# Performance work log

Measured on AMD Instinct MI355X. Metric: run time of the kernel, lower is better.

Reference implementation:

```python
import jax, jax.numpy as jnp
import numpy as np

N = 4096          # samples
D_FEAT = 256      # embedding dim
N_CLASSES = 64
N_NEIGHBORS = 3


def _sq_dists(x):
    # torch.cdist(x, x, p=2).pow(2): squared euclidean pairwise distances
    x2 = jnp.sum(x * x, axis=1)
    d = x2[:, None] + x2[None, :] - 2.0 * (x @ x.T)
    return jnp.maximum(d, 0.0)


def setup_inputs() -> dict:
    key = jax.random.key(0)
    k1, k2 = jax.random.split(key)
    outputs = jax.random.normal(k1, (N, D_FEAT), dtype=jnp.float32)
    label_inds = jax.random.randint(k2, (N,), 0, N_CLASSES)
    return {"outputs": outputs, "label_inds": label_inds, "n_neighbors": N_NEIGHBORS}


def reference(outputs, label_inds, n_neighbors):
    n = outputs.shape[0]
    D = _sq_dists(outputs)                                    # [n, n]

    # _select_targets: per-class k-NN == masked global k-NN (same squared dists)
    same = label_inds[:, None] == label_inds[None, :]
    eye = jnp.eye(n, dtype=bool)
    dd = jnp.where(same & ~eye, D, jnp.inf)
    _, tn = jax.lax.top_k(-dd, n_neighbors)                   # [n, k] target neighbors (global idx)

    target_d = jnp.take_along_axis(D, tn, axis=1)             # [n, k]
    pull = jnp.sum(target_d)
    margin_radii = 1.0 + jnp.max(target_d, axis=1)            # [n]

    # mask: True everywhere except target neighbors and the diagonal
    rows = jnp.arange(n)[:, None]
    mask = jnp.ones((n, n), dtype=bool).at[rows, tn].set(False) & ~eye

    # Original broadcast (max_dist [n,1] vs distance [n,1,n]) yields
    #   push = sum_i sum_{a,j} relu(margin_radii[i] - D[a,j]) * mask[a,j]
    # i.e. each r_i is compared against ALL masked distances. Compute this
    # O(n^3)-element sum exactly in O(n^2 log n) via sort + prefix sums:
    #   sum_d relu(r - d) = r * #{d < r} - sum_{d < r} d
    d_flat = jnp.where(mask.reshape(-1), D.reshape(-1), jnp.inf)
    d_sorted = jnp.sort(d_flat)
    csum = jnp.cumsum(jnp.where(jnp.isinf(d_sorted), 0.0, d_sorted))
    csum0 = jnp.concatenate([jnp.zeros((1,), D.dtype), csum])
    counts = jnp.searchsorted(d_sorted, margin_radii, side='left')  # strict d < r
    push = jnp.sum(margin_radii * counts.astype(D.dtype) - csum0[counts])

    return (pull + push) / n
```

## Files before the change

### kernel.cpp

```cpp
#include <hip/hip_runtime.h>
#include <hip/hip_bf16.h>
#include <float.h>

#define N 4096
#define DF 256
#define NBINS2 4096
#define MAXM 128
#define NPUSHBLK 528

typedef __attribute__((ext_vector_type(8))) short short8v;
typedef __attribute__((ext_vector_type(8))) unsigned short ushort8v;
typedef __attribute__((ext_vector_type(4))) float floatx4;

__device__ inline unsigned short f2bf(float f) {
    __hip_bfloat16 h = __float2bfloat16(f);
    return *reinterpret_cast<unsigned short*>(&h);
}
__device__ inline float bf2f(unsigned short h) {
    unsigned int u = ((unsigned int)h) << 16;
    return __uint_as_float(u);
}

__device__ inline void gload_lds16(const void* g, void* l) {
    __builtin_amdgcn_global_load_lds((const __attribute__((address_space(1))) void*)g,
                                     (__attribute__((address_space(3))) void*)l, 16, 0, 0);
}

__global__ __launch_bounds__(256) void prep_kernel(const float* __restrict__ X,
                                                   const int* __restrict__ labels,
                                                   float* __restrict__ x2,
                                                   __hip_bfloat16* __restrict__ Xb,
                                                   int* __restrict__ cnt,
                                                   int* __restrict__ members,
                                                   double* __restrict__ accd,
                                                   unsigned int* __restrict__ ticket,
                                                   int useXb) {
    int t = threadIdx.x;
    if (blockIdx.x == 1024) {
        __shared__ int scnt[64];
        if (t < 8) accd[t] = 0.0;
        if (t == 8) *ticket = 0u;
        if (t < 64) scnt[t] = 0;
        __syncthreads();
        for (int i = t; i < N; i += 256) {
            int c = labels[i];
            int pos = atomicAdd(&scnt[c], 1);
            if (pos < MAXM) members[(c << 8) + pos] = i;
        }
        __syncthreads();
        if (t < 64) cnt[t] = min(scnt[t], MAXM);
        return;
    }
    int row = blockIdx.x * 4 + (t >> 6);
    int l = t & 63;
    int idx = row * 64 + l;
    float4 v = ((const float4*)X)[idx];
    if (useXb) {
        ushort4 o;
        o.x = f2bf(v.x); o.y = f2bf(v.y); o.z = f2bf(v.z); o.w = f2bf(v.w);
        ((ushort4*)Xb)[idx] = o;
    }
    float s = v.x * v.x + v.y * v.y + v.z * v.z + v.w * v.w;
#pragma unroll
    for (int off = 32; off > 0; off >>= 1) s += __shfl_xor(s, off, 64);
    if (l == 0) x2[row] = s;
}

__device__ inline void top3_upd(float& b0, float& b1, float& b2, float dd) {
    if (dd < b2) {
        if (dd < b1) { b2 = b1; if (dd < b0) { b1 = b0; b0 = dd; } else b1 = dd; }
        else b2 = dd;
    }
}

__global__ __launch_bounds__(512) void knn_mfma_kernel(const float* __restrict__ X,
                                                       const float* __restrict__ x2,
                                                       const int* __restrict__ cnt,
                                                       const int* __restrict__ members,
                                                       float* __restrict__ radii,
                                                       float* __restrict__ targetd) {
    __shared__ __align__(16) char smem[131072];
    __shared__ int marr[MAXM];
    __shared__ float mx2[MAXM];

    int c = blockIdx.x;
    int m = cnt[c];
    int tid = threadIdx.x;
    int lane = tid & 63;
    int wid = tid >> 6;
    const int* mem = members + (c << 8);

    if (tid < MAXM) {
        int mi = (tid < m) ? mem[tid] : -1;
        marr[tid] = mi;
        mx2[tid] = (mi >= 0) ? x2[mi] : 0.f;
    }
    __syncthreads();

    int RB = (m + 15) >> 4;
    char* Hi = smem;
    char* Lo = smem + 65536;

    for (int idx = tid; idx < RB * 512; idx += 512) {
        int rb = idx >> 9;
        int rem = idx & 511;
        int kb = rem >> 4;
        int r0 = rem & 15;
        int row = rb * 16 + r0;
        ushort8v vhi = (ushort8v){0,0,0,0,0,0,0,0};
        ushort8v vlo = vhi;
        if (row < m) {
            const float4* src = (const float4*)(X + (size_t)marr[row] * DF + kb * 8);
            float4 u0 = src[0], u1 = src[1];
            float uu[8] = {u0.x, u0.y, u0.z, u0.w, u1.x, u1.y, u1.z, u1.w};
#pragma unroll
            for (int p = 0; p < 8; ++p) {
                unsigned short h = f2bf(uu[p]);
                vhi[p] = h;
                vlo[p] = f2bf(uu[p] - bf2f(h));
            }
        }
        *((ushort8v*)(Hi + ((size_t)idx << 4))) = vhi;
        *((ushort8v*)(Lo + ((size_t)idx << 4))) = vlo;
    }
    __syncthreads();

    if (wid >= RB) return;

    short8v aHi[8], aLo[8];
#pragma unroll
    for (int kk = 0; kk < 8; ++kk) {
        size_t off = (size_t)wid * 8192 + (size_t)kk * 1024 + ((size_t)lane << 4);
        aHi[kk] = *((const short8v*)(Hi + off));
        aLo[kk] = *((const short8v*)(Lo + off));
    }

    int g = lane >> 4;
    int cl = lane & 15;
    float x2i[4];
#pragma unroll
    for (int r = 0; r < 4; ++r) {
        int il = wid * 16 + g * 4 + r;
        x2i[r] = (il < MAXM) ? mx2[il] : 0.f;
    }

    float t0[4], t1[4], t2[4];
#pragma unroll
    for (int r = 0; r < 4; ++r) { t0[r] = FLT_MAX; t1[r] = FLT_MAX; t2[r] = FLT_MAX; }

    for (int ct = 0; ct < RB; ++ct) {
        floatx4 acc = (floatx4){0.f, 0.f, 0.f, 0.f};
#pragma unroll
        for (int kk = 0; kk < 8; ++kk) {
            size_t off = (size_t)ct * 8192 + (size_t)kk * 1024 + ((size_t)lane << 4);
            short8v bHi = *((const short8v*)(Hi + off));
            short8v bLo = *((const short8v*)(Lo + off));
            acc = __builtin_amdgcn_mfma_f32_16x16x32_bf16(aLo[kk], bHi, acc, 0, 0, 0);
            acc = __builtin_amdgcn_mfma_f32_16x16x32_bf16(aHi[kk], bLo, acc, 0, 0, 0);
            acc = __builtin_amdgcn_mfma_f32_16x16x32_bf16(aHi[kk], bHi, acc, 0, 0, 0);
        }
        int jl = ct * 16 + cl;
        float x2j = (jl < MAXM) ? mx2[jl] : 0.f;
#pragma unroll
        for (int r = 0; r < 4; ++r) {
            int il = wid * 16 + g * 4 + r;
            float d = fmaxf(x2i[r] + x2j - 2.f * acc[r], 0.f);
            bool valid = (jl < m) && (il < m) && (jl != il);
            top3_upd(t0[r], t1[r], t2[r], valid ? d : FLT_MAX);
        }
    }

#pragma unroll
    for (int off = 1; off <= 8; off <<= 1) {
#pragma unroll
        for (int r = 0; r < 4; ++r) {
            float c0 = __shfl_xor(t0[r], off, 64);
            float c1 = __shfl_xor(t1[r], off, 64);
            float c2 = __shfl_xor(t2[r], off, 64);
            float m0, m1, m2;
            if (t0[r] <= c0) {
                m0 = t0[r];
                if (t1[r] <= c0) { m1 = t1[r]; m2 = fminf(t2[r], c0); }
                else { m1 = c0; m2 = fminf(t1[r], c1); }
            } else {
                m0 = c0;
                if (c1 <= t0[r]) { m1 = c1; m2 = fminf(c2, t0[r]); }
                else { m1 = t0[r]; m2 = fminf(c1, t1[r]); }
            }
            t0[r] = m0; t1[r] = m1; t2[r] = m2;
        }
    }
    if (cl == 0) {
#pragma unroll
        for (int r = 0; r < 4; ++r) {
            int il = wid * 16 + g * 4 + r;
            if (il < m) {
                int gi = marr[il];
                targetd[3 * gi + 0] = t0[r];
                targetd[3 * gi + 1] = t1[r];
                targetd[3 * gi + 2] = t2[r];
                radii[gi] = 1.f + t2[r];
            }
        }
    }
}

__global__ __launch_bounds__(1024) void histo_ftab_kernel(const float* __restrict__ radii,
                                                          const float* __restrict__ targetd,
                                                          float2* __restrict__ ftab_g,
                                                          float* __restrict__ hdr,
                                                          double* __restrict__ accd) {
    __shared__ int cntb[NBINS2];
    __shared__ float sumb[NBINS2];
    __shared__ float fv[NBINS2 + 1];
    __shared__ float aux[64];
    __shared__ int iaux[16];
    int t = threadIdx.x;
    int wid = t >> 6, lane = t & 63;

    float4 vv = ((const float4*)radii)[t];
    float v0 = vv.x, v1 = vv.y, v2 = vv.z, v3 = vv.w;

    float mn = fminf(fminf(v0, v1), fminf(v2, v3));
    float mx = fmaxf(fmaxf(v0, v1), fmaxf(v2, v3));
#pragma unroll
    for (int off = 32; off > 0; off >>= 1) {
        mn = fminf(mn, __shfl_xor(mn, off, 64));
        mx = fmaxf(mx, __shfl_xor(mx, off, 64));
    }
    if (lane == 0) { aux[wid] = mn; aux[wid + 16] = mx; }
    cntb[t] = 0; cntb[t + 1024] = 0; cntb[t + 2048] = 0; cntb[t + 3072] = 0;
    sumb[t] = 0.f; sumb[t + 1024] = 0.f; sumb[t + 2048] = 0.f; sumb[t + 3072] = 0.f;
    __syncthreads();
    mn = aux[0]; mx = aux[16];
    for (int w = 1; w < 16; ++w) { mn = fminf(mn, aux[w]); mx = fmaxf(mx, aux[w + 16]); }
    float range = fmaxf(mx - mn, 1e-30f);
    float scale = (float)NBINS2 / range * (1.f - 1e-6f);

    int b0i = max(0, min((int)((v0 - mn) * scale), NBINS2 - 1));
    int b1i = max(0, min((int)((v1 - mn) * scale), NBINS2 - 1));
    int b2i = max(0, min((int)((v2 - mn) * scale), NBINS2 - 1));
    int b3i = max(0, min((int)((v3 - mn) * scale), NBINS2 - 1));
    atomicAdd(&cntb[b0i], 1); atomicAdd(&sumb[b0i], v0);
    atomicAdd(&cntb[b1i], 1); atomicAdd(&sumb[b1i], v1);
    atomicAdd(&cntb[b2i], 1); atomicAdd(&sumb[b2i], v2);
    atomicAdd(&cntb[b3i], 1); atomicAdd(&sumb[b3i], v3);
    __syncthreads();

    int c0 = cntb[4 * t], c1 = cntb[4 * t + 1], c2 = cntb[4 * t + 2], c3 = cntb[4 * t + 3];
    float s0 = sumb[4 * t], s1 = sumb[4 * t + 1], s2 = sumb[4 * t + 2], s3 = sumb[4 * t + 3];
    int toti = c0 + c1 + c2 + c3;
    float totf = s0 + s1 + s2 + s3;
    int sci = toti;
    float scf = totf;
#pragma unroll
    for (int off = 1; off < 64; off <<= 1) {
        int yi = __shfl_down(sci, off, 64);
        float yf = __shfl_down(scf, off, 64);
        if (lane + off < 64) { sci += yi; scf += yf; }
    }
    if (lane == 0) { iaux[wid] = sci; aux[wid] = scf; }
    __syncthreads();
    if (t < 16) {
        int xi = iaux[t];
        float xf = aux[t];
        int si = xi;
        float sf = xf;
#pragma unroll
        for (int off = 1; off < 16; off <<= 1) {
            int yi = __shfl_down(si, off, 64);
            float yf = __shfl_down(sf, off, 64);
            if (t + off < 16) { si += yi; sf += yf; }
        }
        iaux[t] = si - xi;
        aux[t] = sf - xf;
    }
    __syncthreads();
    int afteri = iaux[wid] + (sci - toti);
    float afterf = aux[wid] + (scf - totf);
    int C3 = c3 + afteri, C2 = c2 + C3, C1 = c1 + C2, C0 = c0 + C1;
    float S3 = s3 + afterf, S2 = s2 + S3, S1 = s1 + S2, S0 = s0 + S1;

    float wbin = range / (float)NBINS2;
    {
        float x0 = mn + wbin * (float)(4 * t);
        fv[4 * t + 0] = S0 - x0 * (float)C0;
        float x1 = mn + wbin * (float)(4 * t + 1);
        fv[4 * t + 1] = S1 - x1 * (float)C1;
        float x2e = mn + wbin * (float)(4 * t + 2);
        fv[4 * t + 2] = S2 - x2e * (float)C2;
        float x3 = mn + wbin * (float)(4 * t + 3);
        fv[4 * t + 3] = S3 - x3 * (float)C3;
    }
    if (t == 0) fv[NBINS2] = 0.f;
    __syncthreads();

    for (int b = t; b < NBINS2; b += 1024)
        ftab_g[b] = make_float2(fv[b], fv[b + 1] - fv[b]);
    float Stot = fv[0] + mn * (float)N;
    if (t == 0) {
        hdr[0] = mn;
        hdr[1] = mx;
        hdr[2] = (float)NBINS2 / fmaxf(mx - mn, 1e-20f);
        hdr[3] = Stot;
    }

    float invw = (float)NBINS2 / fmaxf(mx - mn, 1e-20f);
    float loc = 0.f, pul = 0.f;
    for (int idx = t; idx < 3 * N; idx += 1024) {
        float d = targetd[idx];
        pul += d;
        if (d >= mx) continue;
        if (d < mn) {
            loc += fmaf(-d, (float)N, Stot);
        } else {
            float tpos = (d - mn) * invw;
            int b = min((int)tpos, NBINS2 - 1);
            float frac = tpos - (float)b;
            loc += fmaf(frac, fv[b + 1] - fv[b], fv[b]);
        }
    }
#pragma unroll
    for (int off = 32; off > 0; off >>= 1) {
        loc += __shfl_xor(loc, off, 64);
        pul += __shfl_xor(pul, off, 64);
    }
    __syncthreads();
    if (lane == 0) { aux[wid] = loc; aux[wid + 16] = pul; }
    __syncthreads();
    if (t == 0) {
        float s = 0.f, p = 0.f;
        for (int w = 0; w < 16; ++w) { s += aux[w]; p += aux[w + 16]; }
        accd[2] = (double)s;
        accd[0] = (double)p;
    }
}

template<int USEXB>
__global__ __launch_bounds__(256) void push_gemm_kernel(const float* __restrict__ X,
                                                        const __hip_bfloat16* __restrict__ Xb,
                                                        const float* __restrict__ x2,
                                                        const float2* __restrict__ ftab_g,
                                                        const float* __restrict__ hdr,
                                                        float* __restrict__ pp,
                                                        unsigned int* __restrict__ ticket,
                                                        const double* __restrict__ accd,
                                                        float* __restrict__ out) {
    __shared__ __align__(16) char smem[32768];
    __shared__ float x2r[128], x2c[128];
    __shared__ float red[256];
    __shared__ double wsumD[4];
    __shared__ int lastFlag;

    int bid = blockIdx.x;
    int by = 0, rem = bid;
    while (rem >= 32 - by) { rem -= 32 - by; ++by; }
    int bx = by + rem;
    int rowBase = by * 128, colBase = bx * 128;

    int tid = threadIdx.x;
    int lane = tid & 63;
    int wv = tid >> 6;
    int wy = wv >> 1, wx = wv & 1;

    floatx4 acc4[4][4];
#pragma unroll
    for (int m = 0; m < 4; ++m)
#pragma unroll
        for (int n = 0; n < 4; ++n) acc4[m][n] = (floatx4){0.f, 0.f, 0.f, 0.f};

    if (tid < 128) { x2r[tid] = x2[rowBase + tid]; x2c[tid] = x2[colBase + tid]; }

    for (int k0 = 0; k0 < DF; k0 += 64) {
        if (k0) __syncthreads();
        if (USEXB) {
            const __hip_bfloat16* Ab = Xb + (size_t)rowBase * DF;
            const __hip_bfloat16* Bb = Xb + (size_t)colBase * DF;
#pragma unroll
            for (int i = 0; i < 4; ++i) {
                int did = wv * 256 + i * 64 + lane;
                int row = ((did >> 7) << 4) | (did & 15);
                int kb = (did >> 4) & 7;
                size_t goff = (size_t)row * DF + k0 + kb * 8;
                char* ldsA = smem + (size_t)(wv * 256 + i * 64) * 16;
                gload_lds16(Ab + goff, ldsA);
                gload_lds16(Bb + goff, ldsA + 16384);
            }
        } else {
#pragma unroll
            for (int cch = 0; cch < 4; ++cch) {
                int did = tid + (cch << 8);
                int row = ((did >> 7) << 4) | (did & 15);
                int kb = (did >> 4) & 7;
                const float* srcA = X + (size_t)(rowBase + row) * DF + k0 + kb * 8;
                const float* srcB = X + (size_t)(colBase + row) * DF + k0 + kb * 8;
                float4 a0 = *(const float4*)srcA;
                float4 a1 = *(const float4*)(srcA + 4);
                float4 e0 = *(const float4*)srcB;
                float4 e1 = *(const float4*)(srcB + 4);
                ushort8v va, vb;
                va[0] = f2bf(a0.x); va[1] = f2bf(a0.y); va[2] = f2bf(a0.z); va[3] = f2bf(a0.w);
                va[4] = f2bf(a1.x); va[5] = f2bf(a1.y); va[6] = f2bf(a1.z); va[7] = f2bf(a1.w);
                vb[0] = f2bf(e0.x); vb[1] = f2bf(e0.y); vb[2] = f2bf(e0.z); vb[3] = f2bf(e0.w);
                vb[4] = f2bf(e1.x); vb[5] = f2bf(e1.y); vb[6] = f2bf(e1.z); vb[7] = f2bf(e1.w);
                *((ushort8v*)(smem + (did << 4))) = va;
                *((ushort8v*)(smem + 16384 + (did << 4))) = vb;
            }
        }
        __syncthreads();
#pragma unroll
        for (int kk = 0; kk < 2; ++kk) {
            short8v a[4], b[4];
#pragma unroll
            for (int m = 0; m < 4; ++m)
                a[m] = *((const short8v*)(smem + (((wy * 4 + m) * 2 + kk) << 10) + (lane << 4)));
#pragma unroll
            for (int n = 0; n < 4; ++n)
                b[n] = *((const short8v*)(smem + 16384 + (((wx * 4 + n) * 2 + kk) << 10) + (lane << 4)));
#pragma unroll
            for (int m = 0; m < 4; ++m)
#pragma unroll
                for (int n = 0; n < 4; ++n)
                    acc4[m][n] = __builtin_amdgcn_mfma_f32_16x16x32_bf16(a[m], b[n], acc4[m][n], 0, 0, 0);
        }
    }
    __syncthreads();

    float4* ft4 = (float4*)smem;
    for (int i = tid; i < 2048; i += 256) ft4[i] = ((const float4*)ftab_g)[i];
    __syncthreads();
    const float2* ftab = (const float2*)smem;
    float d0v = hdr[0], rmaxv = hdr[1], invw = hdr[2], Stot = hdr[3];
    bool diag = (by == bx);

    float local = 0.f;
    int g = lane >> 4;
    int cl = lane & 15;
#pragma unroll
    for (int m = 0; m < 4; ++m) {
#pragma unroll
        for (int n = 0; n < 4; ++n) {
            floatx4 v = acc4[m][n];
            int gcl = wx * 64 + n * 16 + cl;
            float x2cv = x2c[gcl];
#pragma unroll
            for (int r = 0; r < 4; ++r) {
                int grl = wy * 64 + m * 16 + g * 4 + r;
                if (diag && grl == gcl) continue;
                float d = fmaxf(x2r[grl] + x2cv - 2.f * v[r], 0.f);
                if (d >= rmaxv) continue;
                if (d < d0v) {
                    local += fmaf(-d, (float)N, Stot);
                } else {
                    float tpos = (d - d0v) * invw;
                    int b = min((int)tpos, NBINS2 - 1);
                    float frac = tpos - (float)b;
                    float2 ab = ftab[b];
                    local += fmaf(frac, ab.y, ab.x);
                }
            }
        }
    }
    red[tid] = local;
    __syncthreads();
    for (int s2 = 128; s2 > 0; s2 >>= 1) {
        if (tid < s2) red[tid] += red[tid + s2];
        __syncthreads();
    }
    if (tid == 0) {
        float wt = diag ? 1.f : 2.f;
        pp[bid] = wt * red[0];
        __threadfence();
        unsigned int old = atomicAdd(ticket, 1u);
        lastFlag = (old == NPUSHBLK - 1) ? 1 : 0;
    }
    __syncthreads();

    if (lastFlag) {
        __threadfence();
        double s = 0.0;
        for (int i = tid; i < NPUSHBLK; i += 256) s += (double)pp[i];
#pragma unroll
        for (int off = 32; off > 0; off >>= 1) s += __shfl_down(s, off, 64);
        if (lane == 0) wsumD[wv] = s;
        __syncthreads();
        if (tid == 0) {
            double tot = wsumD[0] + wsumD[1] + wsumD[2] + wsumD[3];
            out[0] = (float)((accd[0] + tot - accd[2]) / (double)N);
        }
    }
}

extern "C" void kernel_launch(void* const* d_in, const int* in_sizes, int n_in,
                              void* d_out, int out_size, void* d_ws, size_t ws_size,
                              hipStream_t stream) {
    const float* X = (const float*)d_in[0];
    const int* labels = (const int*)d_in[1];
    float* out = (float*)d_out;

    char* w = (char*)d_ws;
    double* accd   = (double*)w;
    float* x2      = (float*)(w + 64);
    float* radii   = (float*)(w + 16448);
    float* targetd = (float*)(w + 32832);
    int* cnt       = (int*)(w + 81984);
    int* members   = (int*)(w + 82240);
    float* hdr     = (float*)(w + 147776);
    float2* ftab_g = (float2*)(w + 147840);
    float* pp      = (float*)(w + 180608);
    unsigned int* ticket = (unsigned int*)(w + 182784);
    __hip_bfloat16* Xb = (__hip_bfloat16*)(w + 182848);
    size_t need_xb = 182848 + (size_t)N * DF * 2;
    int useXb = (ws_size >= need_xb) ? 1 : 0;

    hipLaunchKernelGGL(prep_kernel, dim3(1025), dim3(256), 0, stream,
                       X, labels, x2, Xb, cnt, members, accd, ticket, useXb);
    hipLaunchKernelGGL(knn_mfma_kernel, dim3(64), dim3(512), 0, stream,
                       X, x2, cnt, members, radii, targetd);
    hipLaunchKernelGGL(histo_ftab_kernel, dim3(1), dim3(1024), 0, stream,
                       radii, targetd, ftab_g, hdr, accd);
    if (useXb)
        hipLaunchKernelGGL(push_gemm_kernel<1>, dim3(NPUSHBLK), dim3(256), 0, stream,
                           X, Xb, x2, ftab_g, hdr, pp, ticket, accd, out);
    else
        hipLaunchKernelGGL(push_gemm_kernel<0>, dim3(NPUSHBLK), dim3(256), 0, stream,
                           X, Xb, x2, ftab_g, hdr, pp, ticket, accd, out);
}
```

Before: 73.63 us.

## Split per-class kNN across four column-quarter blocks and merge top-3 in histogram kernel

The per-class kNN kernel previously ran one block per class (64 blocks) over the whole class. It now launches 256 blocks, each covering a 32-column slice of the class's members, and writes partial top-3 distances per slice to a workspace buffer. The histogram kernel reads these partials, merges them into the final top-3 and radii, and then builds the histogram. A-operand fragments are now converted directly from global memory instead of LDS, which shrinks shared memory and should let more blocks run at once, at the cost of redundant global reads and a merge step in the single-block histogram kernel.

```diff
diff --git a/kernel.cpp b/kernel.cpp
--- a/kernel.cpp
+++ b/kernel.cpp
@@ -33,13 +33,13 @@
                                                    int* __restrict__ cnt,
                                                    int* __restrict__ members,
                                                    double* __restrict__ accd,
-                                                   unsigned int* __restrict__ ticket,
+                                                   unsigned int* __restrict__ tickets,
                                                    int useXb) {
     int t = threadIdx.x;
     if (blockIdx.x == 1024) {
         __shared__ int scnt[64];
         if (t < 8) accd[t] = 0.0;
-        if (t == 8) *ticket = 0u;
+        if (t == 8) { tickets[0] = 0u; tickets[1] = 0u; }
         if (t < 64) scnt[t] = 0;
         __syncthreads();
         for (int i = t; i < N; i += 256) {
@@ -73,22 +73,24 @@
     }
 }
 
-__global__ __launch_bounds__(512) void knn_mfma_kernel(const float* __restrict__ X,
-                                                       const float* __restrict__ x2,
-                                                       const int* __restrict__ cnt,
-                                                       const int* __restrict__ members,
-                                                       float* __restrict__ radii,
-                                                       float* __restrict__ targetd) {
-    __shared__ __align__(16) char smem[131072];
+__global__ __launch_bounds__(512) void knn4_kernel(const float* __restrict__ X,
+                                                   const float* __restrict__ x2,
+                                                   const int* __restrict__ cnt,
+                                                   const int* __restrict__ members,
+                                                   float* __restrict__ ptop) {
+    __shared__ __align__(16) char smem[32768];
     __shared__ int marr[MAXM];
     __shared__ float mx2[MAXM];
 
-    int c = blockIdx.x;
+    int c = blockIdx.x & 63;
+    int q = blockIdx.x >> 6;
     int m = cnt[c];
+    if (q * 32 >= m) return;
+    const int* mem = members + (c << 8);
     int tid = threadIdx.x;
     int lane = tid & 63;
     int wid = tid >> 6;
-    const int* mem = members + (c << 8);
+    int qbase = q * 32;
 
     if (tid < MAXM) {
         int mi = (tid < m) ? mem[tid] : -1;
@@ -97,20 +99,21 @@
     }
     __syncthreads();
 
-    int RB = (m + 15) >> 4;
     char* Hi = smem;
-    char* Lo = smem + 65536;
-
-    for (int idx = tid; idx < RB * 512; idx += 512) {
+    char* Lo = smem + 16384;
+
+#pragma unroll
+    for (int it = 0; it < 2; ++it) {
+        int idx = it * 512 + tid;
         int rb = idx >> 9;
         int rem = idx & 511;
         int kb = rem >> 4;
         int r0 = rem & 15;
-        int row = rb * 16 + r0;
+        int rg = qbase + rb * 16 + r0;
         ushort8v vhi = (ushort8v){0,0,0,0,0,0,0,0};
         ushort8v vlo = vhi;
-        if (row < m) {
-            const float4* src = (const float4*)(X + (size_t)marr[row] * DF + kb * 8);
+        if (rg < m) {
+            const float4* src = (const float4*)(X + (size_t)marr[rg] * DF + kb * 8);
             float4 u0 = src[0], u1 = src[1];
             float uu[8] = {u0.x, u0.y, u0.z, u0.w, u1.x, u1.y, u1.z, u1.w};
 #pragma unroll
@@ -125,14 +128,32 @@
     }
     __syncthreads();
 
-    if (wid >= RB) return;
-
+    int nstripe = (m + 15) >> 4;
+    if (wid >= nstripe) return;
+
+    int arow = wid * 16 + (lane & 15);
+    bool avalid = (arow < m);
+    const float* aptr = X + (size_t)(avalid ? marr[arow] : 0) * DF;
+    int ko = (lane >> 4) * 8;
     short8v aHi[8], aLo[8];
 #pragma unroll
     for (int kk = 0; kk < 8; ++kk) {
-        size_t off = (size_t)wid * 8192 + (size_t)kk * 1024 + ((size_t)lane << 4);
-        aHi[kk] = *((const short8v*)(Hi + off));
-        aLo[kk] = *((const short8v*)(Lo + off));
+        ushort8v vhi = (ushort8v){0,0,0,0,0,0,0,0};
+        ushort8v vlo = vhi;
+        if (avalid) {
+            const float* p0 = aptr + kk * 32 + ko;
+            float4 u0 = *(const float4*)p0;
+            float4 u1 = *(const float4*)(p0 + 4);
+            float uu[8] = {u0.x, u0.y, u0.z, u0.w, u1.x, u1.y, u1.z, u1.w};
+#pragma unroll
+            for (int p = 0; p < 8; ++p) {
+                unsigned short h = f2bf(uu[p]);
+                vhi[p] = h;
+                vlo[p] = f2bf(uu[p] - bf2f(h));
+            }
+        }
+        aHi[kk] = *(short8v*)&vhi;
+        aLo[kk] = *(short8v*)&vlo;
     }
 
     int g = lane >> 4;
@@ -141,14 +162,15 @@
 #pragma unroll
     for (int r = 0; r < 4; ++r) {
         int il = wid * 16 + g * 4 + r;
-        x2i[r] = (il < MAXM) ? mx2[il] : 0.f;
+        x2i[r] = mx2[il];
     }
 
     float t0[4], t1[4], t2[4];
 #pragma unroll
     for (int r = 0; r < 4; ++r) { t0[r] = FLT_MAX; t1[r] = FLT_MAX; t2[r] = FLT_MAX; }
 
-    for (int ct = 0; ct < RB; ++ct) {
+#pragma unroll
+    for (int ct = 0; ct < 2; ++ct) {
         floatx4 acc = (floatx4){0.f, 0.f, 0.f, 0.f};
 #pragma unroll
         for (int kk = 0; kk < 8; ++kk) {
@@ -159,13 +181,13 @@
             acc = __builtin_amdgcn_mfma_f32_16x16x32_bf16(aHi[kk], bLo, acc, 0, 0, 0);
             acc = __builtin_amdgcn_mfma_f32_16x16x32_bf16(aHi[kk], bHi, acc, 0, 0, 0);
         }
-        int jl = ct * 16 + cl;
-        float x2j = (jl < MAXM) ? mx2[jl] : 0.f;
+        int jg = qbase + ct * 16 + cl;
+        float x2j = (jg < MAXM) ? mx2[jg] : 0.f;
 #pragma unroll
         for (int r = 0; r < 4; ++r) {
             int il = wid * 16 + g * 4 + r;
             float d = fmaxf(x2i[r] + x2j - 2.f * acc[r], 0.f);
-            bool valid = (jl < m) && (il < m) && (jl != il);
+            bool valid = (jg < m) && (il < m) && (jg != il);
             top3_upd(t0[r], t1[r], t2[r], valid ? d : FLT_MAX);
         }
     }
@@ -196,17 +218,16 @@
             int il = wid * 16 + g * 4 + r;
             if (il < m) {
                 int gi = marr[il];
-                targetd[3 * gi + 0] = t0[r];
-                targetd[3 * gi + 1] = t1[r];
-                targetd[3 * gi + 2] = t2[r];
-                radii[gi] = 1.f + t2[r];
-            }
-        }
-    }
-}
-
-__global__ __launch_bounds__(1024) void histo_ftab_kernel(const float* __restrict__ radii,
-                                                          const float* __restrict__ targetd,
+                float* dst = ptop + ((size_t)q * N + gi) * 3;
+                dst[0] = t0[r]; dst[1] = t1[r]; dst[2] = t2[r];
+            }
+        }
+    }
+}
+
+__global__ __launch_bounds__(1024) void histo_ftab_kernel(const int* __restrict__ labels,
+                                                          const int* __restrict__ cnt,
+                                                          const float* __restrict__ ptop,
                                                           float2* __restrict__ ftab_g,
                                                           float* __restrict__ hdr,
                                                           double* __restrict__ accd) {
@@ -218,11 +239,37 @@
     int t = threadIdx.x;
     int wid = t >> 6, lane = t & 63;
 
-    float4 vv = ((const float4*)radii)[t];
-    float v0 = vv.x, v1 = vv.y, v2 = vv.z, v3 = vv.w;
-
-    float mn = fminf(fminf(v0, v1), fminf(v2, v3));
-    float mx = fmaxf(fmaxf(v0, v1), fmaxf(v2, v3));
+    float rad[4];
+    float td[4][3];
+#pragma unroll
+    for (int s = 0; s < 4; ++s) {
+        int i = t + s * 1024;
+        int c = labels[i];
+        int m = cnt[c];
+        int nq = min(4, (m + 31) >> 5);
+        const float* p0 = ptop + (size_t)i * 3;
+        float a0 = p0[0], a1 = p0[1], a2 = p0[2];
+        for (int qq = 1; qq < nq; ++qq) {
+            const float* pq = ptop + ((size_t)qq * N + i) * 3;
+            float b0 = pq[0], b1 = pq[1], b2 = pq[2];
+            float m0, m1, m2;
+            if (a0 <= b0) {
+                m0 = a0;
+                if (a1 <= b0) { m1 = a1; m2 = fminf(a2, b0); }
+                else { m1 = b0; m2 = fminf(a1, b1); }
+            } else {
+                m0 = b0;
+                if (b1 <= a0) { m1 = b1; m2 = fminf(b2, a0); }
+                else { m1 = a0; m2 = fminf(b1, a1); }
+            }
+            a0 = m0; a1 = m1; a2 = m2;
+        }
+        td[s][0] = a0; td[s][1] = a1; td[s][2] = a2;
+        rad[s] = 1.f + a2;
+    }
+
+    float mn = fminf(fminf(rad[0], rad[1]), fminf(rad[2], rad[3]));
+    float mx = fmaxf(fmaxf(rad[0], rad[1]), fmaxf(rad[2], rad[3]));
 #pragma unroll
     for (int off = 32; off > 0; off >>= 1) {
         mn = fminf(mn, __shfl_xor(mn, off, 64));
@@ -237,14 +284,12 @@
     float range = fmaxf(mx - mn, 1e-30f);
     float scale = (float)NBINS2 / range * (1.f - 1e-6f);
 
-    int b0i = max(0, min((int)((v0 - mn) * scale), NBINS2 - 1));
-    int b1i = max(0, min((int)((v1 - mn) * scale), NBINS2 - 1));
-    int b2i = max(0, min((int)((v2 - mn) * scale), NBINS2 - 1));
-    int b3i = max(0, min((int)((v3 - mn) * scale), NBINS2 - 1));
-    atomicAdd(&cntb[b0i], 1); atomicAdd(&sumb[b0i], v0);
-    atomicAdd(&cntb[b1i], 1); atomicAdd(&sumb[b1i], v1);
-    atomicAdd(&cntb[b2i], 1); atomicAdd(&sumb[b2i], v2);
-    atomicAdd(&cntb[b3i], 1); atomicAdd(&sumb[b3i], v3);
+#pragma unroll
+    for (int s = 0; s < 4; ++s) {
+        int b = max(0, min((int)((rad[s] - mn) * scale), NBINS2 - 1));
+        atomicAdd(&cntb[b], 1);
+        atomicAdd(&sumb[b], rad[s]);
+    }
     __syncthreads();
 
     int c0 = cntb[4 * t], c1 = cntb[4 * t + 1], c2 = cntb[4 * t + 2], c3 = cntb[4 * t + 3];
@@ -298,26 +343,30 @@
     for (int b = t; b < NBINS2; b += 1024)
         ftab_g[b] = make_float2(fv[b], fv[b + 1] - fv[b]);
     float Stot = fv[0] + mn * (float)N;
+    float invw = (float)NBINS2 / fmaxf(mx - mn, 1e-20f);
     if (t == 0) {
         hdr[0] = mn;
         hdr[1] = mx;
-        hdr[2] = (float)NBINS2 / fmaxf(mx - mn, 1e-20f);
+        hdr[2] = invw;
         hdr[3] = Stot;
     }
 
-    float invw = (float)NBINS2 / fmaxf(mx - mn, 1e-20f);
     float loc = 0.f, pul = 0.f;
-    for (int idx = t; idx < 3 * N; idx += 1024) {
-        float d = targetd[idx];
-        pul += d;
-        if (d >= mx) continue;
-        if (d < mn) {
-            loc += fmaf(-d, (float)N, Stot);
-        } else {
-            float tpos = (d - mn) * invw;
-            int b = min((int)tpos, NBINS2 - 1);
-            float frac = tpos - (float)b;
-            loc += fmaf(frac, fv[b + 1] - fv[b], fv[b]);
+#pragma unroll
+    for (int s = 0; s < 4; ++s) {
+#pragma unroll
+        for (int k = 0; k < 3; ++k) {
+            float d = td[s][k];
+            pul += d;
+            if (d >= mx) continue;
+            if (d < mn) {
+                loc += fmaf(-d, (float)N, Stot);
+            } else {
+                float tpos = (d - mn) * invw;
+                int b = min((int)tpos, NBINS2 - 1);
+                float frac = tpos - (float)b;
+                loc += fmaf(frac, fv[b + 1] - fv[b], fv[b]);
+            }
         }
     }
 #pragma unroll
@@ -343,7 +392,7 @@
                                                         const float2* __restrict__ ftab_g,
                                                         const float* __restrict__ hdr,
                                                         float* __restrict__ pp,
-                                                        unsigned int* __restrict__ ticket,
+                                                        unsigned int* __restrict__ tickets,
                                                         const double* __restrict__ accd,
                                                         float* __restrict__ out) {
     __shared__ __align__(16) char smem[32768];
@@ -471,7 +520,7 @@
         float wt = diag ? 1.f : 2.f;
         pp[bid] = wt * red[0];
         __threadfence();
-        unsigned int old = atomicAdd(ticket, 1u);
+        unsigned int old = atomicAdd(&tickets[1], 1u);
         lastFlag = (old == NPUSHBLK - 1) ? 1 : 0;
     }
     __syncthreads();
@@ -501,28 +550,27 @@
     char* w = (char*)d_ws;
     double* accd   = (double*)w;
     float* x2      = (float*)(w + 64);
-    float* radii   = (float*)(w + 16448);
-    float* targetd = (float*)(w + 32832);
-    int* cnt       = (int*)(w + 81984);
-    int* members   = (int*)(w + 82240);
-    float* hdr     = (float*)(w + 147776);
-    float2* ftab_g = (float2*)(w + 147840);
-    float* pp      = (float*)(w + 180608);
-    unsigned int* ticket = (unsigned int*)(w + 182784);
-    __hip_bfloat16* Xb = (__hip_bfloat16*)(w + 182848);
-    size_t need_xb = 182848 + (size_t)N * DF * 2;
+    float* ptop    = (float*)(w + 16448);
+    int* cnt       = (int*)(w + 213056);
+    int* members   = (int*)(w + 213312);
+    float* hdr     = (float*)(w + 278848);
+    float2* ftab_g = (float2*)(w + 278912);
+    float* pp      = (float*)(w + 311680);
+    unsigned int* tickets = (unsigned int*)(w + 313792);
+    __hip_bfloat16* Xb = (__hip_bfloat16*)(w + 313856);
+    size_t need_xb = 313856 + (size_t)N * DF * 2;
     int useXb = (ws_size >= need_xb) ? 1 : 0;
 
     hipLaunchKernelGGL(prep_kernel, dim3(1025), dim3(256), 0, stream,
-                       X, labels, x2, Xb, cnt, members, accd, ticket, useXb);
-    hipLaunchKernelGGL(knn_mfma_kernel, dim3(64), dim3(512), 0, stream,
-                       X, x2, cnt, members, radii, targetd);
+                       X, labels, x2, Xb, cnt, members, accd, tickets, useXb);
+    hipLaunchKernelGGL(knn4_kernel, dim3(256), dim3(512), 0, stream,
+                       X, x2, cnt, members, ptop);
     hipLaunchKernelGGL(histo_ftab_kernel, dim3(1), dim3(1024), 0, stream,
-                       radii, targetd, ftab_g, hdr, accd);
+                       labels, cnt, ptop, ftab_g, hdr, accd);
     if (useXb)
         hipLaunchKernelGGL(push_gemm_kernel<1>, dim3(NPUSHBLK), dim3(256), 0, stream,
-                           X, Xb, x2, ftab_g, hdr, pp, ticket, accd, out);
+                           X, Xb, x2, ftab_g, hdr, pp, tickets, accd, out);
     else
         hipLaunchKernelGGL(push_gemm_kernel<0>, dim3(NPUSHBLK), dim3(256), 0, stream,
-                           X, Xb, x2, ftab_g, hdr, pp, ticket, accd, out);
-}
+                           X, Xb, x2, ftab_g, hdr, pp, tickets, accd, out);
+}
```

Result: faster. 67.56 us (-8.3%).
